# Kernel optimization log

Measured on AMD Instinct MI355X. Metric: run time of the kernel, lower is better.

The kernel has to match this reference:

```python
import math
import jax, jax.numpy as jnp
import numpy as np

D = 1024      # d_model
H = 16        # n_heads
HD = 64       # head_dim
DKV = D // 2  # 512
KVHD = DKV // H  # 32
HID = D // 8  # 128 (tau/delta hidden)
B, L, F = 2, 2048, 32


def setup_inputs() -> dict:
    key = jax.random.key(0)
    ks = jax.random.split(key, 16)
    s = 0.02
    return {
        "h": jax.random.normal(ks[0], (B, L, D), jnp.float32),
        "pre_norm_mu": jax.random.normal(ks[1], (B, L, F), jnp.float32),
        "pre_norm_sigma": jax.random.uniform(ks[2], (B, L, F), jnp.float32),
        "Wq": jax.random.normal(ks[3], (D, D), jnp.float32) * s,
        "Wk": jax.random.normal(ks[4], (D, DKV), jnp.float32) * s,
        "Wv": jax.random.normal(ks[5], (D, DKV), jnp.float32) * s,
        "Wo": jax.random.normal(ks[6], (DKV, D), jnp.float32) * s,
        "bo": jnp.zeros((D,), jnp.float32),
        "tau_w1": jax.random.normal(ks[7], (D + 1, HID), jnp.float32) * s,
        "tau_b1": jnp.zeros((HID,), jnp.float32),
        "tau_w2": jax.random.normal(ks[8], (HID, 1), jnp.float32) * s,
        "tau_b2": jnp.zeros((1,), jnp.float32),
        "del_w1": jax.random.normal(ks[9], (D + 1, HID), jnp.float32) * s,
        "del_b1": jnp.zeros((HID,), jnp.float32),
        "del_w2": jax.random.normal(ks[10], (HID, DKV), jnp.float32) * s,
        "del_b2": jnp.zeros((DKV,), jnp.float32),
    }


def _mlp(x, w1, b1, w2, b2):
    # Linear -> exact GELU -> Linear (matches torch nn.GELU default)
    return jax.nn.gelu(x @ w1 + b1, approximate=False) @ w2 + b2


def reference(h, pre_norm_mu, pre_norm_sigma, Wq, Wk, Wv, Wo, bo,
              tau_w1, tau_b1, tau_w2, tau_b2, del_w1, del_b1, del_w2, del_b2):
    b, l, _ = h.shape
    sigma_mean = jnp.clip(pre_norm_sigma.mean(axis=-1, keepdims=True), 1e-6, None)  # (B,L,1)
    mu_mean = pre_norm_mu.mean(axis=-1, keepdims=True)                               # (B,L,1)

    tau = jnp.exp(jnp.clip(_mlp(jnp.concatenate([sigma_mean, h], -1),
                                tau_w1, tau_b1, tau_w2, tau_b2), -3.0, 3.0))  # (B,L,1)
    delta = jnp.clip(_mlp(jnp.concatenate([mu_mean, h], -1),
                          del_w1, del_b1, del_w2, del_b2), -5.0, 5.0)          # (B,L,DKV)

    Q = (h @ Wq).reshape(b, l, H, HD).transpose(0, 2, 1, 3)       # (B,H,L,HD)
    K = (h @ Wk).reshape(b, l, H, KVHD).transpose(0, 2, 1, 3)     # (B,H,L,KVHD)
    V = (h @ Wv).reshape(b, l, H, KVHD).transpose(0, 2, 1, 3)

    Qc = Q[..., :KVHD]                                            # (B,H,L,KVHD)
    logits = jnp.einsum('bhqd,bhkd->bhqk', Qc, K) / math.sqrt(KVHD)
    logits = tau[:, None] * logits                                # tau -> (B,1,L,1): per-query scale

    delta_r = delta.reshape(b, l, H, KVHD).transpose(0, 2, 1, 3)  # (B,H,L,KVHD)
    delta_last = delta_r[:, :, -1, :]                             # (B,H,KVHD)
    delta_bias = jnp.einsum('bhd,bhkd->bhk', delta_last, K)       # (B,H,L_k)
    logits = logits + delta_bias[:, :, None, :]

    logits = jnp.clip(logits, -50.0, 50.0)
    causal = jnp.triu(jnp.ones((l, l), bool), 1)
    logits = jnp.where(causal, -jnp.inf, logits)

    attn = jax.nn.softmax(logits, axis=-1)
    out = jnp.einsum('bhqk,bhkd->bhqd', attn, V)                  # (B,H,L,KVHD)
    out = out.transpose(0, 2, 1, 3).reshape(b, l, DKV)
    out = out @ Wo + bo
    return out[:, -1, :]                                          # (B,D)
```

## Files before the change

kernel.cpp:

```cpp
#include <hip/hip_runtime.h>
#include <hip/hip_bf16.h>

#define Dm   1024
#define Hh   16
#define HDq  64
#define DKV  512
#define HID  128
#define Bb   2
#define Ll   2048
#define Ff   32

typedef _Float16 half8 __attribute__((ext_vector_type(8)));
typedef float f32x4 __attribute__((ext_vector_type(4)));

__device__ __forceinline__ float gelu_exact(float x) {
    return 0.5f * x * (1.0f + erff(x * 0.70710678118654752f));
}

__global__ __launch_bounds__(256) void kpart(
        const float* __restrict__ h, const float* __restrict__ Wq,
        const float* __restrict__ tw1, const float* __restrict__ dw1,
        float* __restrict__ hid_part, float* __restrict__ qc_part)
{
    const int bx = blockIdx.x, t = threadIdx.x;
    __shared__ float hl[32];
    __shared__ float red[256];
    if (bx < 128) {
        const int b = bx >> 6, which = (bx >> 5) & 1, js = bx & 31;
        const float* w1 = which ? dw1 : tw1;
        const float* hrow = h + ((size_t)b * Ll + (Ll - 1)) * Dm + js * 32;
        if (t < 32) hl[t] = hrow[t];
        __syncthreads();
        const int col = t & 127, rg = t >> 7;
        float acc = 0.f;
#pragma unroll
        for (int p = 0; p < 16; ++p) {
            const int row = p * 2 + rg;
            acc += hl[row] * w1[(size_t)(js * 32 + row + 1) * HID + col];
        }
        red[t] = acc;
        __syncthreads();
        if (t < 128)
            hid_part[((size_t)(b * 2 + which) * 32 + js) * HID + t] = red[t] + red[t + 128];
    } else {
        const int id = bx - 128;
        const int b = id >> 5, js = id & 31;
        const float* hrow = h + ((size_t)b * Ll + (Ll - 1)) * Dm + js * 32;
        if (t < 32) hl[t] = hrow[t];
        __syncthreads();
        float4 acc = {0.f, 0.f, 0.f, 0.f};
        const float* Wq0 = Wq + (size_t)(js * 32) * Dm + t * 4;
#pragma unroll
        for (int j = 0; j < 32; ++j) {
            const float x = hl[j];
            float4 wq = *(const float4*)(Wq0 + (size_t)j * Dm);
            acc.x += x * wq.x; acc.y += x * wq.y;
            acc.z += x * wq.z; acc.w += x * wq.w;
        }
        const int col = t * 4;
        if ((col & 63) < 32) {
            const int c = (col >> 6) * 32 + (col & 31);
            *(float4*)(qc_part + ((size_t)b * 32 + js) * DKV + c) = acc;
        }
    }
}

__global__ __launch_bounds__(256) void kkw2(
        const float* __restrict__ mu, const float* __restrict__ sigma,
        const float* __restrict__ tw1, const float* __restrict__ tb1,
        const float* __restrict__ tw2, const float* __restrict__ tb2,
        const float* __restrict__ dw1, const float* __restrict__ db1,
        const float* __restrict__ dw2, const float* __restrict__ db2,
        const float* __restrict__ Wk,
        const float* __restrict__ hid_part, const float* __restrict__ qc_part,
        _Float16* __restrict__ kwh16)
{
    const int jt = blockIdx.x, b = blockIdx.y;
    const int t = threadIdx.x;
    __shared__ float gh[HID];
    __shared__ float red[256];
    __shared__ float wc[DKV];
    __shared__ float kl[16][36];
    __shared__ float s_tau, s_sm, s_mm;

    if (t == 0) {
        float s = 0.f;
        for (int f = 0; f < Ff; ++f) s += sigma[((size_t)b * Ll + (Ll - 1)) * Ff + f];
        s_sm = fmaxf(s / (float)Ff, 1e-6f);
    }
    if (t == 64) {
        float s = 0.f;
        for (int f = 0; f < Ff; ++f) s += mu[((size_t)b * Ll + (Ll - 1)) * Ff + f];
        s_mm = s / (float)Ff;
    }
    __syncthreads();

    if (t < 128) {
        float a = tb1[t] + s_sm * tw1[t];
#pragma unroll
        for (int s = 0; s < 32; ++s)
            a += hid_part[((size_t)(b * 2 + 0) * 32 + s) * HID + t];
        red[t] = gelu_exact(a) * tw2[t];
    } else {
        const int hh = t - 128;
        float a = db1[hh] + s_mm * dw1[hh];
#pragma unroll
        for (int s = 0; s < 32; ++s)
            a += hid_part[((size_t)(b * 2 + 1) * 32 + s) * HID + hh];
        gh[hh] = gelu_exact(a);
        red[t] = 0.f;
    }
    __syncthreads();
    for (int s = 128; s > 0; s >>= 1) {
        if (t < s) red[t] += red[t + s];
        __syncthreads();
    }
    if (t == 0) {
        float s = red[0] + tb2[0];
        s_tau = expf(fminf(fmaxf(s, -3.f), 3.f));
    }
    __syncthreads();

    const int c0 = t, c1 = t + 256;
    float d0 = db2[c0], d1 = db2[c1];
#pragma unroll 16
    for (int i = 0; i < HID; ++i) {
        const float x = gh[i];
        d0 += x * dw2[(size_t)i * DKV + c0];
        d1 += x * dw2[(size_t)i * DKV + c1];
    }
    d0 = fminf(fmaxf(d0, -5.f), 5.f);
    d1 = fminf(fmaxf(d1, -5.f), 5.f);
    float q0 = 0.f, q1 = 0.f;
#pragma unroll
    for (int s = 0; s < 32; ++s) {
        const float* qp = qc_part + ((size_t)b * 32 + s) * DKV;
        q0 += qp[c0];
        q1 += qp[c1];
    }
    const float inv_sqrt = 0.17677669529663687f;
    wc[c0] = s_tau * q0 * inv_sqrt + d0;
    wc[c1] = s_tau * q1 * inv_sqrt + d1;
    __syncthreads();

    const float w0 = wc[t * 2], w1 = wc[t * 2 + 1];
    const int hd = t >> 4;
#pragma unroll 4
    for (int jj = 0; jj < 32; ++jj) {
        const int j = jt * 32 + jj;
        float2 kv = *(const float2*)(Wk + (size_t)j * DKV + t * 2);
        float p = kv.x * w0 + kv.y * w1;
        p += __shfl_xor(p, 1); p += __shfl_xor(p, 2);
        p += __shfl_xor(p, 4); p += __shfl_xor(p, 8);
        if ((t & 15) == 0) kl[hd][jj] = p;
    }
    __syncthreads();
    if (t < 64) {
        const int head = t & 15, jl = (t >> 4) * 8;
        half8 v;
#pragma unroll
        for (int e = 0; e < 8; ++e) v[e] = (_Float16)kl[head][jl + e];
        *(half8*)(kwh16 + ((size_t)(b * 32 + jt)) * 512 + t * 8) = v;
    }
}

__global__ __launch_bounds__(512) void kmid(
        const float* __restrict__ h, const _Float16* __restrict__ kwh16,
        float* __restrict__ den_part, float* __restrict__ hbar_part)
{
    __shared__ __align__(16) _Float16 Kw[16384];
    __shared__ float lred[8][32][17];
    __shared__ float p_lds[32][16];
    const int rt = blockIdx.x, b = blockIdx.y;
    const int t = threadIdx.x;
    const int w = t >> 6, l = t & 63;
    const int rows0 = (b * 64 + rt) * 32;

#pragma unroll
    for (int i = 0; i < 4; ++i) {
        const int idx = i * 512 + t;
        *(half8*)(Kw + idx * 8) = *(const half8*)(kwh16 + (size_t)b * 16384 + idx * 8);
    }
    __syncthreads();

    f32x4 lacc[2] = {};
    const float* ap = h + (size_t)(rows0 + (l & 15)) * Dm + (l >> 4) * 8;
#pragma unroll
    for (int mt = 0; mt < 2; ++mt) {
        const float* apm = ap + (size_t)mt * 16 * Dm;
#pragma unroll
        for (int ks = 0; ks < 4; ++ks) {
            const int kt = w * 4 + ks;
            float4 x0 = *(const float4*)(apm + kt * 32);
            float4 x1 = *(const float4*)(apm + kt * 32 + 4);
            half8 af;
            af[0] = (_Float16)x0.x; af[1] = (_Float16)x0.y; af[2] = (_Float16)x0.z; af[3] = (_Float16)x0.w;
            af[4] = (_Float16)x1.x; af[5] = (_Float16)x1.y; af[6] = (_Float16)x1.z; af[7] = (_Float16)x1.w;
            half8 kf = *(const half8*)(Kw + kt * 512 + l * 8);
            lacc[mt] = __builtin_amdgcn_mfma_f32_16x16x32_f16(af, kf, lacc[mt], 0, 0, 0);
        }
    }
#pragma unroll
    for (int mt = 0; mt < 2; ++mt)
#pragma unroll
        for (int r = 0; r < 4; ++r)
            lred[w][mt * 16 + (l >> 4) * 4 + r][l & 15] = lacc[mt][r];
    __syncthreads();

    {
        const int row = t >> 4, head = t & 15;
        float val = 0.f;
#pragma unroll
        for (int ww = 0; ww < 8; ++ww) val += lred[ww][row][head];
        val = fminf(fmaxf(val, -50.f), 50.f);
        p_lds[row][head] = __expf(val - 50.f);
    }
    __syncthreads();

    if (t < 16) {
        float s = 0.f;
#pragma unroll
        for (int r = 0; r < 32; ++r) s += p_lds[r][t];
        den_part[((size_t)b * Hh + t) * 64 + rt] = s;
    }

    const int j0 = (t & 127) * 8;
    const int h0 = (t >> 7) * 4;
    f32x4 acc2[2][4] = {};
#pragma unroll 4
    for (int l2 = 0; l2 < 32; ++l2) {
        const float* hr = h + (size_t)(rows0 + l2) * Dm + j0;
        f32x4 hv0 = *(const f32x4*)hr;
        f32x4 hv1 = *(const f32x4*)(hr + 4);
        f32x4 pp = *(const f32x4*)(&p_lds[l2][h0]);
#pragma unroll
        for (int hh = 0; hh < 4; ++hh) {
            acc2[0][hh] += hv0 * pp[hh];
            acc2[1][hh] += hv1 * pp[hh];
        }
    }
#pragma unroll
    for (int hh = 0; hh < 4; ++hh) {
        float* dst = hbar_part + ((size_t)(b * 64 + rt) * Hh + h0 + hh) * Dm + j0;
        *(f32x4*)dst = acc2[0][hh];
        *(f32x4*)(dst + 4) = acc2[1][hh];
    }
}

__global__ __launch_bounds__(256) void kopre(
        const float* __restrict__ hbar_part, const float* __restrict__ Wv,
        float* __restrict__ opre_part)
{
    const int hd = blockIdx.x, b = blockIdx.y, js = blockIdx.z;
    const int t = threadIdx.x;
    __shared__ f32x4 pA[32][8];
    __shared__ float hb[128];
    __shared__ float red[256];

    const int slot = t >> 3, rs = t & 7;
    f32x4 a = {};
#pragma unroll
    for (int i = 0; i < 8; ++i) {
        const int rt = rs + i * 8;
        a += *(const f32x4*)(hbar_part + ((size_t)(b * 64 + rt) * Hh + hd) * Dm + js * 128 + slot * 4);
    }
    pA[slot][rs] = a;
    __syncthreads();
    if (t < 32) {
        f32x4 s = {};
#pragma unroll
        for (int r = 0; r < 8; ++r) s += pA[t][r];
        *(f32x4*)(hb + t * 4) = s;
    }
    __syncthreads();

    const int c = t & 31, jg = t >> 5;
    float acc = 0.f;
#pragma unroll
    for (int i = 0; i < 16; ++i)
        acc += hb[jg * 16 + i] * Wv[(size_t)(js * 128 + jg * 16 + i) * DKV + hd * 32 + c];
    red[t] = acc;
    __syncthreads();
    if (t < 32) {
        float s = 0.f;
#pragma unroll
        for (int g = 0; g < 8; ++g) s += red[g * 32 + t];
        opre_part[((size_t)(b * Hh + hd) * 8 + js) * 32 + t] = s;
    }
}

__global__ __launch_bounds__(256) void kout(
        const float* __restrict__ opre_part, const float* __restrict__ den_part,
        const float* __restrict__ Wo, const float* __restrict__ bo,
        float* __restrict__ out)
{
    const int nt = blockIdx.x, b = blockIdx.y;
    const int t = threadIdx.x;
    __shared__ float op[DKV];
    __shared__ float den_s[16];
    __shared__ float red[256];

    if (t < 16) {
        float s = 0.f;
#pragma unroll 16
        for (int rt = 0; rt < 64; ++rt)
            s += den_part[((size_t)b * Hh + t) * 64 + rt];
        den_s[t] = s;
    }
    __syncthreads();
#pragma unroll
    for (int cc = 0; cc < 2; ++cc) {
        const int c = cc * 256 + t;
        float s = 0.f;
#pragma unroll
        for (int js = 0; js < 8; ++js)
            s += opre_part[((size_t)(b * Hh + (c >> 5)) * 8 + js) * 32 + (c & 31)];
        op[c] = s / den_s[c >> 5];
    }
    __syncthreads();

    const int nl = t & 31, cg = t >> 5;
    const int n = nt * 32 + nl;
    float acc = 0.f;
#pragma unroll 16
    for (int c = cg * 64; c < cg * 64 + 64; ++c)
        acc += op[c] * Wo[(size_t)c * Dm + n];
    red[t] = acc;
    __syncthreads();
    if (t < 32) {
        float s = 0.f;
#pragma unroll
        for (int g = 0; g < 8; ++g) s += red[g * 32 + t];
        out[(size_t)b * Dm + nt * 32 + t] = bo[nt * 32 + t] + s;
    }
}

extern "C" void kernel_launch(void* const* d_in, const int* in_sizes, int n_in,
                              void* d_out, int out_size, void* d_ws, size_t ws_size,
                              hipStream_t stream) {
    const float* h      = (const float*)d_in[0];
    const float* mu     = (const float*)d_in[1];
    const float* sigma  = (const float*)d_in[2];
    const float* Wq     = (const float*)d_in[3];
    const float* Wk     = (const float*)d_in[4];
    const float* Wv     = (const float*)d_in[5];
    const float* Wo     = (const float*)d_in[6];
    const float* bo     = (const float*)d_in[7];
    const float* tau_w1 = (const float*)d_in[8];
    const float* tau_b1 = (const float*)d_in[9];
    const float* tau_w2 = (const float*)d_in[10];
    const float* tau_b2 = (const float*)d_in[11];
    const float* del_w1 = (const float*)d_in[12];
    const float* del_b1 = (const float*)d_in[13];
    const float* del_w2 = (const float*)d_in[14];
    const float* del_b2 = (const float*)d_in[15];
    float* out = (float*)d_out;

    _Float16* kwh16  = (_Float16*)d_ws;
    float* den_part  = (float*)(kwh16 + 32768);
    float* hid_part  = den_part + 2048;
    float* qc_part   = hid_part + 16384;
    float* opre_part = qc_part + 32768;
    float* hbar_part = opre_part + 8192;

    kpart<<<192, 256, 0, stream>>>(h, Wq, tau_w1, del_w1, hid_part, qc_part);
    kkw2<<<dim3(32, Bb), 256, 0, stream>>>(mu, sigma, tau_w1, tau_b1, tau_w2, tau_b2,
                                           del_w1, del_b1, del_w2, del_b2, Wk,
                                           hid_part, qc_part, kwh16);
    kmid<<<dim3(64, Bb), 512, 0, stream>>>(h, kwh16, den_part, hbar_part);
    kopre<<<dim3(16, Bb, 8), 256, 0, stream>>>(hbar_part, Wv, opre_part);
    kout<<<dim3(32, Bb), 256, 0, stream>>>(opre_part, den_part, Wo, bo, out);
}
```

Measured before the change: 52.04 us.

## Fuse five kernels into one persistent kernel with global atomic barriers

Merges the five stage kernels into a single 256-block kernel whose phases are separated by spin-wait grid barriers on atomic counters, which are zeroed by a memset before launch. The goal is to remove the per-launch overhead and the idle gaps between small dependent kernels. The middle stage now runs with 256 threads instead of 512, so each thread does more k-steps and wider hbar accumulation. The design relies on all 256 blocks being resident at once to avoid deadlock, and adds atomic polling and fence costs at each barrier.

After: 171.5 us. 230% more time.

```diff
diff --git a/kernel.cpp b/kernel.cpp
--- a/kernel.cpp
+++ b/kernel.cpp
@@ -9,6 +9,7 @@
 #define Bb   2
 #define Ll   2048
 #define Ff   32
+#define NBLK 256
 
 typedef _Float16 half8 __attribute__((ext_vector_type(8)));
 typedef float f32x4 __attribute__((ext_vector_type(4)));
@@ -17,321 +18,330 @@
     return 0.5f * x * (1.0f + erff(x * 0.70710678118654752f));
 }
 
-__global__ __launch_bounds__(256) void kpart(
-        const float* __restrict__ h, const float* __restrict__ Wq,
-        const float* __restrict__ tw1, const float* __restrict__ dw1,
-        float* __restrict__ hid_part, float* __restrict__ qc_part)
-{
-    const int bx = blockIdx.x, t = threadIdx.x;
-    __shared__ float hl[32];
-    __shared__ float red[256];
-    if (bx < 128) {
-        const int b = bx >> 6, which = (bx >> 5) & 1, js = bx & 31;
-        const float* w1 = which ? dw1 : tw1;
-        const float* hrow = h + ((size_t)b * Ll + (Ll - 1)) * Dm + js * 32;
-        if (t < 32) hl[t] = hrow[t];
-        __syncthreads();
-        const int col = t & 127, rg = t >> 7;
-        float acc = 0.f;
-#pragma unroll
-        for (int p = 0; p < 16; ++p) {
-            const int row = p * 2 + rg;
-            acc += hl[row] * w1[(size_t)(js * 32 + row + 1) * HID + col];
-        }
-        red[t] = acc;
-        __syncthreads();
-        if (t < 128)
-            hid_part[((size_t)(b * 2 + which) * 32 + js) * HID + t] = red[t] + red[t + 128];
-    } else {
-        const int id = bx - 128;
-        const int b = id >> 5, js = id & 31;
-        const float* hrow = h + ((size_t)b * Ll + (Ll - 1)) * Dm + js * 32;
-        if (t < 32) hl[t] = hrow[t];
-        __syncthreads();
-        float4 acc = {0.f, 0.f, 0.f, 0.f};
-        const float* Wq0 = Wq + (size_t)(js * 32) * Dm + t * 4;
-#pragma unroll
-        for (int j = 0; j < 32; ++j) {
-            const float x = hl[j];
-            float4 wq = *(const float4*)(Wq0 + (size_t)j * Dm);
-            acc.x += x * wq.x; acc.y += x * wq.y;
-            acc.z += x * wq.z; acc.w += x * wq.w;
-        }
-        const int col = t * 4;
-        if ((col & 63) < 32) {
-            const int c = (col >> 6) * 32 + (col & 31);
-            *(float4*)(qc_part + ((size_t)b * 32 + js) * DKV + c) = acc;
-        }
-    }
+__device__ __forceinline__ void gbar(int* c) {
+    __syncthreads();
+    if (threadIdx.x == 0) {
+        __threadfence();
+        atomicAdd(c, 1);
+        while (atomicAdd(c, 0) < NBLK) __builtin_amdgcn_s_sleep(8);
+    }
+    __syncthreads();
+    __threadfence();
 }
 
-__global__ __launch_bounds__(256) void kkw2(
+__global__ __launch_bounds__(256) void kfused(
+        const float* __restrict__ h,
         const float* __restrict__ mu, const float* __restrict__ sigma,
+        const float* __restrict__ Wq, const float* __restrict__ Wk,
+        const float* __restrict__ Wv, const float* __restrict__ Wo,
+        const float* __restrict__ bo,
         const float* __restrict__ tw1, const float* __restrict__ tb1,
         const float* __restrict__ tw2, const float* __restrict__ tb2,
         const float* __restrict__ dw1, const float* __restrict__ db1,
         const float* __restrict__ dw2, const float* __restrict__ db2,
-        const float* __restrict__ Wk,
-        const float* __restrict__ hid_part, const float* __restrict__ qc_part,
-        _Float16* __restrict__ kwh16)
-{
-    const int jt = blockIdx.x, b = blockIdx.y;
-    const int t = threadIdx.x;
-    __shared__ float gh[HID];
-    __shared__ float red[256];
-    __shared__ float wc[DKV];
-    __shared__ float kl[16][36];
-    __shared__ float s_tau, s_sm, s_mm;
-
-    if (t == 0) {
-        float s = 0.f;
-        for (int f = 0; f < Ff; ++f) s += sigma[((size_t)b * Ll + (Ll - 1)) * Ff + f];
-        s_sm = fmaxf(s / (float)Ff, 1e-6f);
-    }
-    if (t == 64) {
-        float s = 0.f;
-        for (int f = 0; f < Ff; ++f) s += mu[((size_t)b * Ll + (Ll - 1)) * Ff + f];
-        s_mm = s / (float)Ff;
-    }
-    __syncthreads();
-
-    if (t < 128) {
-        float a = tb1[t] + s_sm * tw1[t];
-#pragma unroll
-        for (int s = 0; s < 32; ++s)
-            a += hid_part[((size_t)(b * 2 + 0) * 32 + s) * HID + t];
-        red[t] = gelu_exact(a) * tw2[t];
-    } else {
-        const int hh = t - 128;
-        float a = db1[hh] + s_mm * dw1[hh];
-#pragma unroll
-        for (int s = 0; s < 32; ++s)
-            a += hid_part[((size_t)(b * 2 + 1) * 32 + s) * HID + hh];
-        gh[hh] = gelu_exact(a);
-        red[t] = 0.f;
-    }
-    __syncthreads();
-    for (int s = 128; s > 0; s >>= 1) {
-        if (t < s) red[t] += red[t + s];
-        __syncthreads();
-    }
-    if (t == 0) {
-        float s = red[0] + tb2[0];
-        s_tau = expf(fminf(fmaxf(s, -3.f), 3.f));
-    }
-    __syncthreads();
-
-    const int c0 = t, c1 = t + 256;
-    float d0 = db2[c0], d1 = db2[c1];
-#pragma unroll 16
-    for (int i = 0; i < HID; ++i) {
-        const float x = gh[i];
-        d0 += x * dw2[(size_t)i * DKV + c0];
-        d1 += x * dw2[(size_t)i * DKV + c1];
-    }
-    d0 = fminf(fmaxf(d0, -5.f), 5.f);
-    d1 = fminf(fmaxf(d1, -5.f), 5.f);
-    float q0 = 0.f, q1 = 0.f;
-#pragma unroll
-    for (int s = 0; s < 32; ++s) {
-        const float* qp = qc_part + ((size_t)b * 32 + s) * DKV;
-        q0 += qp[c0];
-        q1 += qp[c1];
-    }
-    const float inv_sqrt = 0.17677669529663687f;
-    wc[c0] = s_tau * q0 * inv_sqrt + d0;
-    wc[c1] = s_tau * q1 * inv_sqrt + d1;
-    __syncthreads();
-
-    const float w0 = wc[t * 2], w1 = wc[t * 2 + 1];
-    const int hd = t >> 4;
-#pragma unroll 4
-    for (int jj = 0; jj < 32; ++jj) {
-        const int j = jt * 32 + jj;
-        float2 kv = *(const float2*)(Wk + (size_t)j * DKV + t * 2);
-        float p = kv.x * w0 + kv.y * w1;
-        p += __shfl_xor(p, 1); p += __shfl_xor(p, 2);
-        p += __shfl_xor(p, 4); p += __shfl_xor(p, 8);
-        if ((t & 15) == 0) kl[hd][jj] = p;
-    }
-    __syncthreads();
-    if (t < 64) {
-        const int head = t & 15, jl = (t >> 4) * 8;
-        half8 v;
-#pragma unroll
-        for (int e = 0; e < 8; ++e) v[e] = (_Float16)kl[head][jl + e];
-        *(half8*)(kwh16 + ((size_t)(b * 32 + jt)) * 512 + t * 8) = v;
-    }
-}
-
-__global__ __launch_bounds__(512) void kmid(
-        const float* __restrict__ h, const _Float16* __restrict__ kwh16,
-        float* __restrict__ den_part, float* __restrict__ hbar_part)
-{
-    __shared__ __align__(16) _Float16 Kw[16384];
-    __shared__ float lred[8][32][17];
-    __shared__ float p_lds[32][16];
-    const int rt = blockIdx.x, b = blockIdx.y;
-    const int t = threadIdx.x;
-    const int w = t >> 6, l = t & 63;
-    const int rows0 = (b * 64 + rt) * 32;
-
-#pragma unroll
-    for (int i = 0; i < 4; ++i) {
-        const int idx = i * 512 + t;
-        *(half8*)(Kw + idx * 8) = *(const half8*)(kwh16 + (size_t)b * 16384 + idx * 8);
-    }
-    __syncthreads();
-
-    f32x4 lacc[2] = {};
-    const float* ap = h + (size_t)(rows0 + (l & 15)) * Dm + (l >> 4) * 8;
-#pragma unroll
-    for (int mt = 0; mt < 2; ++mt) {
-        const float* apm = ap + (size_t)mt * 16 * Dm;
-#pragma unroll
-        for (int ks = 0; ks < 4; ++ks) {
-            const int kt = w * 4 + ks;
-            float4 x0 = *(const float4*)(apm + kt * 32);
-            float4 x1 = *(const float4*)(apm + kt * 32 + 4);
-            half8 af;
-            af[0] = (_Float16)x0.x; af[1] = (_Float16)x0.y; af[2] = (_Float16)x0.z; af[3] = (_Float16)x0.w;
-            af[4] = (_Float16)x1.x; af[5] = (_Float16)x1.y; af[6] = (_Float16)x1.z; af[7] = (_Float16)x1.w;
-            half8 kf = *(const half8*)(Kw + kt * 512 + l * 8);
-            lacc[mt] = __builtin_amdgcn_mfma_f32_16x16x32_f16(af, kf, lacc[mt], 0, 0, 0);
-        }
-    }
-#pragma unroll
-    for (int mt = 0; mt < 2; ++mt)
-#pragma unroll
-        for (int r = 0; r < 4; ++r)
-            lred[w][mt * 16 + (l >> 4) * 4 + r][l & 15] = lacc[mt][r];
-    __syncthreads();
-
-    {
-        const int row = t >> 4, head = t & 15;
-        float val = 0.f;
-#pragma unroll
-        for (int ww = 0; ww < 8; ++ww) val += lred[ww][row][head];
-        val = fminf(fmaxf(val, -50.f), 50.f);
-        p_lds[row][head] = __expf(val - 50.f);
-    }
-    __syncthreads();
-
-    if (t < 16) {
-        float s = 0.f;
-#pragma unroll
-        for (int r = 0; r < 32; ++r) s += p_lds[r][t];
-        den_part[((size_t)b * Hh + t) * 64 + rt] = s;
-    }
-
-    const int j0 = (t & 127) * 8;
-    const int h0 = (t >> 7) * 4;
-    f32x4 acc2[2][4] = {};
-#pragma unroll 4
-    for (int l2 = 0; l2 < 32; ++l2) {
-        const float* hr = h + (size_t)(rows0 + l2) * Dm + j0;
-        f32x4 hv0 = *(const f32x4*)hr;
-        f32x4 hv1 = *(const f32x4*)(hr + 4);
-        f32x4 pp = *(const f32x4*)(&p_lds[l2][h0]);
-#pragma unroll
-        for (int hh = 0; hh < 4; ++hh) {
-            acc2[0][hh] += hv0 * pp[hh];
-            acc2[1][hh] += hv1 * pp[hh];
-        }
-    }
-#pragma unroll
-    for (int hh = 0; hh < 4; ++hh) {
-        float* dst = hbar_part + ((size_t)(b * 64 + rt) * Hh + h0 + hh) * Dm + j0;
-        *(f32x4*)dst = acc2[0][hh];
-        *(f32x4*)(dst + 4) = acc2[1][hh];
-    }
-}
-
-__global__ __launch_bounds__(256) void kopre(
-        const float* __restrict__ hbar_part, const float* __restrict__ Wv,
-        float* __restrict__ opre_part)
-{
-    const int hd = blockIdx.x, b = blockIdx.y, js = blockIdx.z;
-    const int t = threadIdx.x;
-    __shared__ f32x4 pA[32][8];
-    __shared__ float hb[128];
-    __shared__ float red[256];
-
-    const int slot = t >> 3, rs = t & 7;
-    f32x4 a = {};
-#pragma unroll
-    for (int i = 0; i < 8; ++i) {
-        const int rt = rs + i * 8;
-        a += *(const f32x4*)(hbar_part + ((size_t)(b * 64 + rt) * Hh + hd) * Dm + js * 128 + slot * 4);
-    }
-    pA[slot][rs] = a;
-    __syncthreads();
-    if (t < 32) {
-        f32x4 s = {};
-#pragma unroll
-        for (int r = 0; r < 8; ++r) s += pA[t][r];
-        *(f32x4*)(hb + t * 4) = s;
-    }
-    __syncthreads();
-
-    const int c = t & 31, jg = t >> 5;
-    float acc = 0.f;
-#pragma unroll
-    for (int i = 0; i < 16; ++i)
-        acc += hb[jg * 16 + i] * Wv[(size_t)(js * 128 + jg * 16 + i) * DKV + hd * 32 + c];
-    red[t] = acc;
-    __syncthreads();
-    if (t < 32) {
-        float s = 0.f;
-#pragma unroll
-        for (int g = 0; g < 8; ++g) s += red[g * 32 + t];
-        opre_part[((size_t)(b * Hh + hd) * 8 + js) * 32 + t] = s;
-    }
-}
-
-__global__ __launch_bounds__(256) void kout(
-        const float* __restrict__ opre_part, const float* __restrict__ den_part,
-        const float* __restrict__ Wo, const float* __restrict__ bo,
+        int* __restrict__ counters,
+        _Float16* __restrict__ kwh16, float* __restrict__ den_part,
+        float* __restrict__ hid_part, float* __restrict__ qc_part,
+        float* __restrict__ opre_part, float* __restrict__ hbar_part,
         float* __restrict__ out)
 {
-    const int nt = blockIdx.x, b = blockIdx.y;
-    const int t = threadIdx.x;
-    __shared__ float op[DKV];
-    __shared__ float den_s[16];
-    __shared__ float red[256];
-
-    if (t < 16) {
-        float s = 0.f;
+    __shared__ __align__(16) char sm[44544];
+    const int bx = blockIdx.x, t = threadIdx.x;
+
+    if (bx < 192) {
+        float* hl  = (float*)sm;
+        float* red = (float*)(sm + 128);
+        if (bx < 128) {
+            const int b = bx >> 6, which = (bx >> 5) & 1, js = bx & 31;
+            const float* w1 = which ? dw1 : tw1;
+            const float* hrow = h + ((size_t)b * Ll + (Ll - 1)) * Dm + js * 32;
+            if (t < 32) hl[t] = hrow[t];
+            __syncthreads();
+            const int col = t & 127, rg = t >> 7;
+            float acc = 0.f;
+#pragma unroll
+            for (int p = 0; p < 16; ++p) {
+                const int row = p * 2 + rg;
+                acc += hl[row] * w1[(size_t)(js * 32 + row + 1) * HID + col];
+            }
+            red[t] = acc;
+            __syncthreads();
+            if (t < 128)
+                hid_part[((size_t)(b * 2 + which) * 32 + js) * HID + t] = red[t] + red[t + 128];
+        } else {
+            const int id = bx - 128;
+            const int b = id >> 5, js = id & 31;
+            const float* hrow = h + ((size_t)b * Ll + (Ll - 1)) * Dm + js * 32;
+            if (t < 32) hl[t] = hrow[t];
+            __syncthreads();
+            float4 acc = {0.f, 0.f, 0.f, 0.f};
+            const float* Wq0 = Wq + (size_t)(js * 32) * Dm + t * 4;
+#pragma unroll
+            for (int j = 0; j < 32; ++j) {
+                const float x = hl[j];
+                float4 wq = *(const float4*)(Wq0 + (size_t)j * Dm);
+                acc.x += x * wq.x; acc.y += x * wq.y;
+                acc.z += x * wq.z; acc.w += x * wq.w;
+            }
+            const int col = t * 4;
+            if ((col & 63) < 32) {
+                const int c = (col >> 6) * 32 + (col & 31);
+                *(float4*)(qc_part + ((size_t)b * 32 + js) * DKV + c) = acc;
+            }
+        }
+    }
+    gbar(counters + 0);
+
+    if (bx < 64) {
+        float* gh  = (float*)sm;
+        float* red = (float*)(sm + 512);
+        float* wc  = (float*)(sm + 1536);
+        float (*kl)[36] = (float(*)[36])(sm + 3584);
+        float* scal = (float*)(sm + 5888);
+        const int jt = bx & 31, b = bx >> 5;
+
+        if (t == 0) {
+            float s = 0.f;
+            for (int f = 0; f < Ff; ++f) s += sigma[((size_t)b * Ll + (Ll - 1)) * Ff + f];
+            scal[1] = fmaxf(s / (float)Ff, 1e-6f);
+        }
+        if (t == 64) {
+            float s = 0.f;
+            for (int f = 0; f < Ff; ++f) s += mu[((size_t)b * Ll + (Ll - 1)) * Ff + f];
+            scal[2] = s / (float)Ff;
+        }
+        __syncthreads();
+
+        if (t < 128) {
+            float a = tb1[t] + scal[1] * tw1[t];
+#pragma unroll
+            for (int s = 0; s < 32; ++s)
+                a += hid_part[((size_t)(b * 2 + 0) * 32 + s) * HID + t];
+            red[t] = gelu_exact(a) * tw2[t];
+        } else {
+            const int hh = t - 128;
+            float a = db1[hh] + scal[2] * dw1[hh];
+#pragma unroll
+            for (int s = 0; s < 32; ++s)
+                a += hid_part[((size_t)(b * 2 + 1) * 32 + s) * HID + hh];
+            gh[hh] = gelu_exact(a);
+            red[t] = 0.f;
+        }
+        __syncthreads();
+        for (int s = 128; s > 0; s >>= 1) {
+            if (t < s) red[t] += red[t + s];
+            __syncthreads();
+        }
+        if (t == 0) {
+            float s = red[0] + tb2[0];
+            scal[0] = expf(fminf(fmaxf(s, -3.f), 3.f));
+        }
+        __syncthreads();
+
+        const int c0 = t, c1 = t + 256;
+        float d0 = db2[c0], d1 = db2[c1];
 #pragma unroll 16
-        for (int rt = 0; rt < 64; ++rt)
-            s += den_part[((size_t)b * Hh + t) * 64 + rt];
-        den_s[t] = s;
-    }
-    __syncthreads();
-#pragma unroll
-    for (int cc = 0; cc < 2; ++cc) {
-        const int c = cc * 256 + t;
-        float s = 0.f;
-#pragma unroll
-        for (int js = 0; js < 8; ++js)
-            s += opre_part[((size_t)(b * Hh + (c >> 5)) * 8 + js) * 32 + (c & 31)];
-        op[c] = s / den_s[c >> 5];
-    }
-    __syncthreads();
-
-    const int nl = t & 31, cg = t >> 5;
-    const int n = nt * 32 + nl;
-    float acc = 0.f;
+        for (int i = 0; i < HID; ++i) {
+            const float x = gh[i];
+            d0 += x * dw2[(size_t)i * DKV + c0];
+            d1 += x * dw2[(size_t)i * DKV + c1];
+        }
+        d0 = fminf(fmaxf(d0, -5.f), 5.f);
+        d1 = fminf(fmaxf(d1, -5.f), 5.f);
+        float q0 = 0.f, q1 = 0.f;
+#pragma unroll
+        for (int s = 0; s < 32; ++s) {
+            const float* qp = qc_part + ((size_t)b * 32 + s) * DKV;
+            q0 += qp[c0];
+            q1 += qp[c1];
+        }
+        const float inv_sqrt = 0.17677669529663687f;
+        wc[c0] = scal[0] * q0 * inv_sqrt + d0;
+        wc[c1] = scal[0] * q1 * inv_sqrt + d1;
+        __syncthreads();
+
+        const float w0 = wc[t * 2], w1v = wc[t * 2 + 1];
+        const int hd = t >> 4;
+#pragma unroll 4
+        for (int jj = 0; jj < 32; ++jj) {
+            const int j = jt * 32 + jj;
+            float2 kv = *(const float2*)(Wk + (size_t)j * DKV + t * 2);
+            float p = kv.x * w0 + kv.y * w1v;
+            p += __shfl_xor(p, 1); p += __shfl_xor(p, 2);
+            p += __shfl_xor(p, 4); p += __shfl_xor(p, 8);
+            if ((t & 15) == 0) kl[hd][jj] = p;
+        }
+        __syncthreads();
+        if (t < 64) {
+            const int head = t & 15, jl = (t >> 4) * 8;
+            half8 v;
+#pragma unroll
+            for (int e = 0; e < 8; ++e) v[e] = (_Float16)kl[head][jl + e];
+            *(half8*)(kwh16 + ((size_t)(b * 32 + jt)) * 512 + t * 8) = v;
+        }
+    }
+    gbar(counters + 1);
+
+    if (bx < 128) {
+        _Float16* Kw = (_Float16*)sm;
+        float (*lred)[32][17] = (float(*)[32][17])(sm + 32768);
+        float (*p_lds)[16] = (float(*)[16])(sm + 41472);
+        const int b = bx >> 6, rt = bx & 63;
+        const int w = t >> 6, l = t & 63;
+        const int rows0 = (b * 64 + rt) * 32;
+
+#pragma unroll
+        for (int i = 0; i < 8; ++i) {
+            const int idx = i * 256 + t;
+            *(half8*)(Kw + idx * 8) = *(const half8*)(kwh16 + (size_t)b * 16384 + idx * 8);
+        }
+        __syncthreads();
+
+        f32x4 lacc[2] = {};
+        const float* ap = h + (size_t)(rows0 + (l & 15)) * Dm + (l >> 4) * 8;
+#pragma unroll
+        for (int mt = 0; mt < 2; ++mt) {
+            const float* apm = ap + (size_t)mt * 16 * Dm;
+#pragma unroll
+            for (int ks = 0; ks < 8; ++ks) {
+                const int kt = w * 8 + ks;
+                float4 x0 = *(const float4*)(apm + kt * 32);
+                float4 x1 = *(const float4*)(apm + kt * 32 + 4);
+                half8 af;
+                af[0] = (_Float16)x0.x; af[1] = (_Float16)x0.y; af[2] = (_Float16)x0.z; af[3] = (_Float16)x0.w;
+                af[4] = (_Float16)x1.x; af[5] = (_Float16)x1.y; af[6] = (_Float16)x1.z; af[7] = (_Float16)x1.w;
+                half8 kf = *(const half8*)(Kw + kt * 512 + l * 8);
+                lacc[mt] = __builtin_amdgcn_mfma_f32_16x16x32_f16(af, kf, lacc[mt], 0, 0, 0);
+            }
+        }
+#pragma unroll
+        for (int mt = 0; mt < 2; ++mt)
+#pragma unroll
+            for (int r = 0; r < 4; ++r)
+                lred[w][mt * 16 + (l >> 4) * 4 + r][l & 15] = lacc[mt][r];
+        __syncthreads();
+
+#pragma unroll
+        for (int i = 0; i < 2; ++i) {
+            const int row = i * 16 + (t >> 4), head = t & 15;
+            float val = lred[0][row][head] + lred[1][row][head]
+                      + lred[2][row][head] + lred[3][row][head];
+            val = fminf(fmaxf(val, -50.f), 50.f);
+            p_lds[row][head] = __expf(val - 50.f);
+        }
+        __syncthreads();
+
+        if (t < 16) {
+            float s = 0.f;
+#pragma unroll
+            for (int r = 0; r < 32; ++r) s += p_lds[r][t];
+            den_part[((size_t)b * Hh + t) * 64 + rt] = s;
+        }
+
+        const int j0 = (t & 63) * 16;
+        const int h0 = (t >> 6) * 4;
+        f32x4 acc2[4][4] = {};
+#pragma unroll 8
+        for (int l2 = 0; l2 < 32; ++l2) {
+            const float* hr = h + (size_t)(rows0 + l2) * Dm + j0;
+            f32x4 hv[4];
+#pragma unroll
+            for (int jj = 0; jj < 4; ++jj) hv[jj] = *(const f32x4*)(hr + jj * 4);
+            f32x4 pp = *(const f32x4*)(&p_lds[l2][h0]);
+#pragma unroll
+            for (int hh = 0; hh < 4; ++hh)
+#pragma unroll
+                for (int jj = 0; jj < 4; ++jj)
+                    acc2[jj][hh] += hv[jj] * pp[hh];
+        }
+#pragma unroll
+        for (int hh = 0; hh < 4; ++hh) {
+            float* dst = hbar_part + ((size_t)(b * 64 + rt) * Hh + h0 + hh) * Dm + j0;
+#pragma unroll
+            for (int jj = 0; jj < 4; ++jj)
+                *(f32x4*)(dst + jj * 4) = acc2[jj][hh];
+        }
+    }
+    gbar(counters + 2);
+
+    {
+        f32x4 (*pA)[8] = (f32x4(*)[8])sm;
+        float* hb  = (float*)(sm + 4096);
+        float* red = (float*)(sm + 4608);
+        const int hd = bx & 15, b = (bx >> 4) & 1, js = bx >> 5;
+
+        const int slot = t >> 3, rs = t & 7;
+        f32x4 a = {};
+#pragma unroll
+        for (int i = 0; i < 8; ++i) {
+            const int rt = rs + i * 8;
+            a += *(const f32x4*)(hbar_part + ((size_t)(b * 64 + rt) * Hh + hd) * Dm + js * 128 + slot * 4);
+        }
+        pA[slot][rs] = a;
+        __syncthreads();
+        if (t < 32) {
+            f32x4 s = {};
+#pragma unroll
+            for (int r = 0; r < 8; ++r) s += pA[t][r];
+            *(f32x4*)(hb + t * 4) = s;
+        }
+        __syncthreads();
+
+        const int c = t & 31, jg = t >> 5;
+        float acc = 0.f;
+#pragma unroll
+        for (int i = 0; i < 16; ++i)
+            acc += hb[jg * 16 + i] * Wv[(size_t)(js * 128 + jg * 16 + i) * DKV + hd * 32 + c];
+        red[t] = acc;
+        __syncthreads();
+        if (t < 32) {
+            float s = 0.f;
+#pragma unroll
+            for (int g = 0; g < 8; ++g) s += red[g * 32 + t];
+            opre_part[((size_t)(b * Hh + hd) * 8 + js) * 32 + t] = s;
+        }
+    }
+    gbar(counters + 3);
+
+    if (bx < 64) {
+        float* op    = (float*)sm;
+        float* den_s = (float*)(sm + 2048);
+        float* red   = (float*)(sm + 2176);
+        const int nt = bx & 31, b = bx >> 5;
+
+        if (t < 16) {
+            float s = 0.f;
 #pragma unroll 16
-    for (int c = cg * 64; c < cg * 64 + 64; ++c)
-        acc += op[c] * Wo[(size_t)c * Dm + n];
-    red[t] = acc;
-    __syncthreads();
-    if (t < 32) {
-        float s = 0.f;
-#pragma unroll
-        for (int g = 0; g < 8; ++g) s += red[g * 32 + t];
-        out[(size_t)b * Dm + nt * 32 + t] = bo[nt * 32 + t] + s;
+            for (int rt = 0; rt < 64; ++rt)
+                s += den_part[((size_t)b * Hh + t) * 64 + rt];
+            den_s[t] = s;
+        }
+        __syncthreads();
+#pragma unroll
+        for (int cc = 0; cc < 2; ++cc) {
+            const int c = cc * 256 + t;
+            float s = 0.f;
+#pragma unroll
+            for (int js = 0; js < 8; ++js)
+                s += opre_part[((size_t)(b * Hh + (c >> 5)) * 8 + js) * 32 + (c & 31)];
+            op[c] = s / den_s[c >> 5];
+        }
+        __syncthreads();
+
+        const int nl = t & 31, cg = t >> 5;
+        const int n = nt * 32 + nl;
+        float acc = 0.f;
+#pragma unroll 16
+        for (int c = cg * 64; c < cg * 64 + 64; ++c)
+            acc += op[c] * Wo[(size_t)c * Dm + n];
+        red[t] = acc;
+        __syncthreads();
+        if (t < 32) {
+            float s = 0.f;
+#pragma unroll
+            for (int g = 0; g < 8; ++g) s += red[g * 32 + t];
+            out[(size_t)b * Dm + nt * 32 + t] = bo[nt * 32 + t] + s;
+        }
     }
 }
 
@@ -356,18 +366,18 @@
     const float* del_b2 = (const float*)d_in[15];
     float* out = (float*)d_out;
 
-    _Float16* kwh16  = (_Float16*)d_ws;
+    int* counters    = (int*)d_ws;
+    _Float16* kwh16  = (_Float16*)((char*)d_ws + 64);
     float* den_part  = (float*)(kwh16 + 32768);
     float* hid_part  = den_part + 2048;
     float* qc_part   = hid_part + 16384;
     float* opre_part = qc_part + 32768;
     float* hbar_part = opre_part + 8192;
 
-    kpart<<<192, 256, 0, stream>>>(h, Wq, tau_w1, del_w1, hid_part, qc_part);
-    kkw2<<<dim3(32, Bb), 256, 0, stream>>>(mu, sigma, tau_w1, tau_b1, tau_w2, tau_b2,
-                                           del_w1, del_b1, del_w2, del_b2, Wk,
-                                           hid_part, qc_part, kwh16);
-    kmid<<<dim3(64, Bb), 512, 0, stream>>>(h, kwh16, den_part, hbar_part);
-    kopre<<<dim3(16, Bb, 8), 256, 0, stream>>>(hbar_part, Wv, opre_part);
-    kout<<<dim3(32, Bb), 256, 0, stream>>>(opre_part, den_part, Wo, bo, out);
+    hipMemsetAsync(counters, 0, 64, stream);
+    kfused<<<NBLK, 256, 0, stream>>>(h, mu, sigma, Wq, Wk, Wv, Wo, bo,
+                                     tau_w1, tau_b1, tau_w2, tau_b2,
+                                     del_w1, del_b1, del_w2, del_b2,
+                                     counters, kwh16, den_part, hid_part,
+                                     qc_part, opre_part, hbar_part, out);
 }
```

## Share weight loads across batches and split kmid into smaller row tiles

Applied to the files above, without the earlier changes.

kpart and kout now handle both batch elements in one block, so each weight element (tau/delta W1, Wq, Wo) is loaded once and applied to two rows. This halves the weight traffic and block count for those kernels. kmid moves from 32-row tiles with 512 threads to 16-row tiles with 256 threads and twice as many blocks, raising parallelism across CUs. In exchange, kmid's hbar_part partials double in size, which adds memory traffic in kopre and more partial-sum work there. Each kmid block also reloads the whole 32KB Kw tile into LDS.

Measured after the change: 56.13 us. 1.08x slower.

```diff
diff --git a/kernel.cpp b/kernel.cpp
--- a/kernel.cpp
+++ b/kernel.cpp
@@ -23,44 +23,48 @@
         float* __restrict__ hid_part, float* __restrict__ qc_part)
 {
     const int bx = blockIdx.x, t = threadIdx.x;
-    __shared__ float hl[32];
-    __shared__ float red[256];
-    if (bx < 128) {
-        const int b = bx >> 6, which = (bx >> 5) & 1, js = bx & 31;
+    __shared__ float hl0[32], hl1[32];
+    __shared__ float red0[256], red1[256];
+    if (bx < 64) {
+        const int which = bx >> 5, js = bx & 31;
         const float* w1 = which ? dw1 : tw1;
-        const float* hrow = h + ((size_t)b * Ll + (Ll - 1)) * Dm + js * 32;
-        if (t < 32) hl[t] = hrow[t];
+        if (t < 32)       hl0[t]      = h[((size_t)0 * Ll + (Ll - 1)) * Dm + js * 32 + t];
+        else if (t < 64)  hl1[t - 32] = h[((size_t)1 * Ll + (Ll - 1)) * Dm + js * 32 + (t - 32)];
         __syncthreads();
         const int col = t & 127, rg = t >> 7;
-        float acc = 0.f;
+        float a0 = 0.f, a1 = 0.f;
 #pragma unroll
         for (int p = 0; p < 16; ++p) {
             const int row = p * 2 + rg;
-            acc += hl[row] * w1[(size_t)(js * 32 + row + 1) * HID + col];
+            const float w = w1[(size_t)(js * 32 + row + 1) * HID + col];
+            a0 += hl0[row] * w;
+            a1 += hl1[row] * w;
         }
-        red[t] = acc;
+        red0[t] = a0; red1[t] = a1;
         __syncthreads();
-        if (t < 128)
-            hid_part[((size_t)(b * 2 + which) * 32 + js) * HID + t] = red[t] + red[t + 128];
+        if (t < 128) {
+            hid_part[((size_t)(0 * 2 + which) * 32 + js) * HID + t] = red0[t] + red0[t + 128];
+            hid_part[((size_t)(1 * 2 + which) * 32 + js) * HID + t] = red1[t] + red1[t + 128];
+        }
     } else {
-        const int id = bx - 128;
-        const int b = id >> 5, js = id & 31;
-        const float* hrow = h + ((size_t)b * Ll + (Ll - 1)) * Dm + js * 32;
-        if (t < 32) hl[t] = hrow[t];
+        const int js = bx - 64;
+        if (t < 32)       hl0[t]      = h[((size_t)0 * Ll + (Ll - 1)) * Dm + js * 32 + t];
+        else if (t < 64)  hl1[t - 32] = h[((size_t)1 * Ll + (Ll - 1)) * Dm + js * 32 + (t - 32)];
         __syncthreads();
-        float4 acc = {0.f, 0.f, 0.f, 0.f};
+        float4 a0 = {0.f, 0.f, 0.f, 0.f}, a1 = {0.f, 0.f, 0.f, 0.f};
         const float* Wq0 = Wq + (size_t)(js * 32) * Dm + t * 4;
 #pragma unroll
         for (int j = 0; j < 32; ++j) {
-            const float x = hl[j];
             float4 wq = *(const float4*)(Wq0 + (size_t)j * Dm);
-            acc.x += x * wq.x; acc.y += x * wq.y;
-            acc.z += x * wq.z; acc.w += x * wq.w;
+            const float x0 = hl0[j], x1 = hl1[j];
+            a0.x += x0 * wq.x; a0.y += x0 * wq.y; a0.z += x0 * wq.z; a0.w += x0 * wq.w;
+            a1.x += x1 * wq.x; a1.y += x1 * wq.y; a1.z += x1 * wq.z; a1.w += x1 * wq.w;
         }
         const int col = t * 4;
         if ((col & 63) < 32) {
             const int c = (col >> 6) * 32 + (col & 31);
-            *(float4*)(qc_part + ((size_t)b * 32 + js) * DKV + c) = acc;
+            *(float4*)(qc_part + ((size_t)0 * 32 + js) * DKV + c) = a0;
+            *(float4*)(qc_part + ((size_t)1 * 32 + js) * DKV + c) = a1;
         }
     }
 }
@@ -143,13 +147,13 @@
     wc[c1] = s_tau * q1 * inv_sqrt + d1;
     __syncthreads();
 
-    const float w0 = wc[t * 2], w1 = wc[t * 2 + 1];
+    const float w0 = wc[t * 2], w1v = wc[t * 2 + 1];
     const int hd = t >> 4;
 #pragma unroll 4
     for (int jj = 0; jj < 32; ++jj) {
         const int j = jt * 32 + jj;
         float2 kv = *(const float2*)(Wk + (size_t)j * DKV + t * 2);
-        float p = kv.x * w0 + kv.y * w1;
+        float p = kv.x * w0 + kv.y * w1v;
         p += __shfl_xor(p, 1); p += __shfl_xor(p, 2);
         p += __shfl_xor(p, 4); p += __shfl_xor(p, 8);
         if ((t & 15) == 0) kl[hd][jj] = p;
@@ -164,54 +168,47 @@
     }
 }
 
-__global__ __launch_bounds__(512) void kmid(
+__global__ __launch_bounds__(256) void kmid(
         const float* __restrict__ h, const _Float16* __restrict__ kwh16,
         float* __restrict__ den_part, float* __restrict__ hbar_part)
 {
     __shared__ __align__(16) _Float16 Kw[16384];
-    __shared__ float lred[8][32][17];
-    __shared__ float p_lds[32][16];
+    __shared__ float lred[4][16][17];
+    __shared__ float p_lds[16][16];
     const int rt = blockIdx.x, b = blockIdx.y;
     const int t = threadIdx.x;
     const int w = t >> 6, l = t & 63;
-    const int rows0 = (b * 64 + rt) * 32;
-
-#pragma unroll
-    for (int i = 0; i < 4; ++i) {
-        const int idx = i * 512 + t;
+    const int rows0 = (b * 128 + rt) * 16;
+
+#pragma unroll
+    for (int i = 0; i < 8; ++i) {
+        const int idx = i * 256 + t;
         *(half8*)(Kw + idx * 8) = *(const half8*)(kwh16 + (size_t)b * 16384 + idx * 8);
     }
     __syncthreads();
 
-    f32x4 lacc[2] = {};
+    f32x4 lacc = {};
     const float* ap = h + (size_t)(rows0 + (l & 15)) * Dm + (l >> 4) * 8;
 #pragma unroll
-    for (int mt = 0; mt < 2; ++mt) {
-        const float* apm = ap + (size_t)mt * 16 * Dm;
-#pragma unroll
-        for (int ks = 0; ks < 4; ++ks) {
-            const int kt = w * 4 + ks;
-            float4 x0 = *(const float4*)(apm + kt * 32);
-            float4 x1 = *(const float4*)(apm + kt * 32 + 4);
-            half8 af;
-            af[0] = (_Float16)x0.x; af[1] = (_Float16)x0.y; af[2] = (_Float16)x0.z; af[3] = (_Float16)x0.w;
-            af[4] = (_Float16)x1.x; af[5] = (_Float16)x1.y; af[6] = (_Float16)x1.z; af[7] = (_Float16)x1.w;
-            half8 kf = *(const half8*)(Kw + kt * 512 + l * 8);
-            lacc[mt] = __builtin_amdgcn_mfma_f32_16x16x32_f16(af, kf, lacc[mt], 0, 0, 0);
-        }
-    }
-#pragma unroll
-    for (int mt = 0; mt < 2; ++mt)
-#pragma unroll
-        for (int r = 0; r < 4; ++r)
-            lred[w][mt * 16 + (l >> 4) * 4 + r][l & 15] = lacc[mt][r];
+    for (int ks = 0; ks < 8; ++ks) {
+        const int kt = w * 8 + ks;
+        float4 x0 = *(const float4*)(ap + kt * 32);
+        float4 x1 = *(const float4*)(ap + kt * 32 + 4);
+        half8 af;
+        af[0] = (_Float16)x0.x; af[1] = (_Float16)x0.y; af[2] = (_Float16)x0.z; af[3] = (_Float16)x0.w;
+        af[4] = (_Float16)x1.x; af[5] = (_Float16)x1.y; af[6] = (_Float16)x1.z; af[7] = (_Float16)x1.w;
+        half8 kf = *(const half8*)(Kw + kt * 512 + l * 8);
+        lacc = __builtin_amdgcn_mfma_f32_16x16x32_f16(af, kf, lacc, 0, 0, 0);
+    }
+#pragma unroll
+    for (int r = 0; r < 4; ++r)
+        lred[w][(l >> 4) * 4 + r][l & 15] = lacc[r];
     __syncthreads();
 
     {
         const int row = t >> 4, head = t & 15;
-        float val = 0.f;
-#pragma unroll
-        for (int ww = 0; ww < 8; ++ww) val += lred[ww][row][head];
+        float val = lred[0][row][head] + lred[1][row][head]
+                  + lred[2][row][head] + lred[3][row][head];
         val = fminf(fmaxf(val, -50.f), 50.f);
         p_lds[row][head] = __expf(val - 50.f);
     }
@@ -220,30 +217,32 @@
     if (t < 16) {
         float s = 0.f;
 #pragma unroll
-        for (int r = 0; r < 32; ++r) s += p_lds[r][t];
-        den_part[((size_t)b * Hh + t) * 64 + rt] = s;
-    }
-
-    const int j0 = (t & 127) * 8;
-    const int h0 = (t >> 7) * 4;
-    f32x4 acc2[2][4] = {};
+        for (int r = 0; r < 16; ++r) s += p_lds[r][t];
+        den_part[((size_t)b * Hh + t) * 128 + rt] = s;
+    }
+
+    const int j0 = (t & 63) * 16;
+    const int h0 = (t >> 6) * 4;
+    f32x4 acc2[4][4] = {};
 #pragma unroll 4
-    for (int l2 = 0; l2 < 32; ++l2) {
+    for (int l2 = 0; l2 < 16; ++l2) {
         const float* hr = h + (size_t)(rows0 + l2) * Dm + j0;
-        f32x4 hv0 = *(const f32x4*)hr;
-        f32x4 hv1 = *(const f32x4*)(hr + 4);
+        f32x4 hv[4];
+#pragma unroll
+        for (int jj = 0; jj < 4; ++jj) hv[jj] = *(const f32x4*)(hr + jj * 4);
         f32x4 pp = *(const f32x4*)(&p_lds[l2][h0]);
 #pragma unroll
-        for (int hh = 0; hh < 4; ++hh) {
-            acc2[0][hh] += hv0 * pp[hh];
-            acc2[1][hh] += hv1 * pp[hh];
-        }
+        for (int hh = 0; hh < 4; ++hh)
+#pragma unroll
+            for (int jj = 0; jj < 4; ++jj)
+                acc2[jj][hh] += hv[jj] * pp[hh];
     }
 #pragma unroll
     for (int hh = 0; hh < 4; ++hh) {
-        float* dst = hbar_part + ((size_t)(b * 64 + rt) * Hh + h0 + hh) * Dm + j0;
-        *(f32x4*)dst = acc2[0][hh];
-        *(f32x4*)(dst + 4) = acc2[1][hh];
+        float* dst = hbar_part + ((size_t)(b * 128 + rt) * Hh + h0 + hh) * Dm + j0;
+#pragma unroll
+        for (int jj = 0; jj < 4; ++jj)
+            *(f32x4*)(dst + jj * 4) = acc2[jj][hh];
     }
 }
 
@@ -260,9 +259,9 @@
     const int slot = t >> 3, rs = t & 7;
     f32x4 a = {};
 #pragma unroll
-    for (int i = 0; i < 8; ++i) {
+    for (int i = 0; i < 16; ++i) {
         const int rt = rs + i * 8;
-        a += *(const f32x4*)(hbar_part + ((size_t)(b * 64 + rt) * Hh + hd) * Dm + js * 128 + slot * 4);
+        a += *(const f32x4*)(hbar_part + ((size_t)(b * 128 + rt) * Hh + hd) * Dm + js * 128 + slot * 4);
     }
     pA[slot][rs] = a;
     __syncthreads();
@@ -294,44 +293,59 @@
         const float* __restrict__ Wo, const float* __restrict__ bo,
         float* __restrict__ out)
 {
-    const int nt = blockIdx.x, b = blockIdx.y;
+    const int nt = blockIdx.x;
     const int t = threadIdx.x;
-    __shared__ float op[DKV];
-    __shared__ float den_s[16];
-    __shared__ float red[256];
-
-    if (t < 16) {
-        float s = 0.f;
-#pragma unroll 16
-        for (int rt = 0; rt < 64; ++rt)
-            s += den_part[((size_t)b * Hh + t) * 64 + rt];
-        den_s[t] = s;
-    }
-    __syncthreads();
-#pragma unroll
-    for (int cc = 0; cc < 2; ++cc) {
-        const int c = cc * 256 + t;
+    __shared__ float op[2][DKV];
+    __shared__ float dred[32][8];
+    __shared__ float den_s[2][16];
+    __shared__ float red0[256], red1[256];
+
+    {
+        const int b = t >> 7, hd = (t >> 3) & 15, rg = t & 7;
+        float s = 0.f;
+#pragma unroll
+        for (int i = 0; i < 16; ++i)
+            s += den_part[((size_t)b * Hh + hd) * 128 + rg + i * 8];
+        dred[b * 16 + hd][rg] = s;
+    }
+    __syncthreads();
+    if (t < 32) {
+        float s = 0.f;
+#pragma unroll
+        for (int g = 0; g < 8; ++g) s += dred[t][g];
+        den_s[t >> 4][t & 15] = s;
+    }
+    __syncthreads();
+#pragma unroll
+    for (int cc = 0; cc < 4; ++cc) {
+        const int idx = cc * 256 + t;
+        const int b = idx >> 9, c = idx & 511;
         float s = 0.f;
 #pragma unroll
         for (int js = 0; js < 8; ++js)
             s += opre_part[((size_t)(b * Hh + (c >> 5)) * 8 + js) * 32 + (c & 31)];
-        op[c] = s / den_s[c >> 5];
+        op[b][c] = s / den_s[b][c >> 5];
     }
     __syncthreads();
 
     const int nl = t & 31, cg = t >> 5;
     const int n = nt * 32 + nl;
-    float acc = 0.f;
+    float a0 = 0.f, a1 = 0.f;
 #pragma unroll 16
-    for (int c = cg * 64; c < cg * 64 + 64; ++c)
-        acc += op[c] * Wo[(size_t)c * Dm + n];
-    red[t] = acc;
+    for (int c = cg * 64; c < cg * 64 + 64; ++c) {
+        const float wv = Wo[(size_t)c * Dm + n];
+        a0 += op[0][c] * wv;
+        a1 += op[1][c] * wv;
+    }
+    red0[t] = a0; red1[t] = a1;
     __syncthreads();
     if (t < 32) {
-        float s = 0.f;
-#pragma unroll
-        for (int g = 0; g < 8; ++g) s += red[g * 32 + t];
-        out[(size_t)b * Dm + nt * 32 + t] = bo[nt * 32 + t] + s;
+        float s0 = 0.f, s1 = 0.f;
+#pragma unroll
+        for (int g = 0; g < 8; ++g) { s0 += red0[g * 32 + t]; s1 += red1[g * 32 + t]; }
+        const float bv = bo[nt * 32 + t];
+        out[(size_t)0 * Dm + nt * 32 + t] = bv + s0;
+        out[(size_t)1 * Dm + nt * 32 + t] = bv + s1;
     }
 }
 
@@ -358,16 +372,16 @@
 
     _Float16* kwh16  = (_Float16*)d_ws;
     float* den_part  = (float*)(kwh16 + 32768);
-    float* hid_part  = den_part + 2048;
+    float* hid_part  = den_part + 4096;
     float* qc_part   = hid_part + 16384;
     float* opre_part = qc_part + 32768;
     float* hbar_part = opre_part + 8192;
 
-    kpart<<<192, 256, 0, stream>>>(h, Wq, tau_w1, del_w1, hid_part, qc_part);
+    kpart<<<96, 256, 0, stream>>>(h, Wq, tau_w1, del_w1, hid_part, qc_part);
     kkw2<<<dim3(32, Bb), 256, 0, stream>>>(mu, sigma, tau_w1, tau_b1, tau_w2, tau_b2,
                                            del_w1, del_b1, del_w2, del_b2, Wk,
                                            hid_part, qc_part, kwh16);
-    kmid<<<dim3(64, Bb), 512, 0, stream>>>(h, kwh16, den_part, hbar_part);
+    kmid<<<dim3(128, Bb), 256, 0, stream>>>(h, kwh16, den_part, hbar_part);
     kopre<<<dim3(16, Bb, 8), 256, 0, stream>>>(hbar_part, Wv, opre_part);
-    kout<<<dim3(32, Bb), 256, 0, stream>>>(opre_part, den_part, Wo, bo, out);
-}
+    kout<<<32, 256, 0, stream>>>(opre_part, den_part, Wo, bo, out);
+}
```
